# Kernel optimization log

Hardware: AMD Instinct MI355X
Metric: run time of the kernel (lower is better)

## Reference

```python
import jax, jax.numpy as jnp
import numpy as np

N = 100000      # nodes
E = 1600000     # edges
FX = 128        # raw node feature dim
MAXZ = 100      # z embedding / one-hot size
HID = 128       # hidden_channels
NL = 3          # num_layers
G = 512         # num graphs
BN_EPS = 1e-5


def _lin(key, din, dout):
    return jax.random.normal(key, (din, dout), jnp.float32) * (1.0 / np.sqrt(din))


def setup_inputs() -> dict:
    key = jax.random.key(0)
    ks = jax.random.split(key, 64)
    d = {}
    d["x"] = jax.random.normal(ks[0], (N, FX), jnp.float32)
    d["z"] = jax.random.randint(ks[1], (N,), 0, MAXZ)
    d["edge_index"] = jax.random.randint(ks[2], (2, E), 0, N)
    d["batch"] = jnp.sort(jax.random.randint(ks[3], (N,), 0, G))
    in0 = FX + 2 * MAXZ  # z_emb concatenated twice (faithful to source)
    ki = 4
    for l in range(NL):
        din = in0 if l == 0 else HID
        d[f"W1_{l}"] = _lin(ks[ki], din, HID); ki += 1
        d[f"b1_{l}"] = jnp.zeros((HID,), jnp.float32)
        d[f"W2_{l}"] = _lin(ks[ki], HID, HID); ki += 1
        d[f"b2_{l}"] = jnp.zeros((HID,), jnp.float32)
        d[f"g_{l}"] = jnp.ones((HID,), jnp.float32)
        d[f"be_{l}"] = jnp.zeros((HID,), jnp.float32)
    d["Wl1"] = _lin(ks[ki], NL * HID, HID); ki += 1
    d["bl1"] = jnp.zeros((HID,), jnp.float32)
    d["Wl2"] = _lin(ks[ki], HID, 1); ki += 1
    d["bl2"] = jnp.zeros((1,), jnp.float32)
    return d


def _gin_layer(h, src, dst, W1, b1, W2, b2, g, be):
    # GINConv with eps=0: nn(x + sum_{j->i} x_j)
    agg = jax.ops.segment_sum(h[src], dst, num_segments=N)  # [N, d]
    m = h + agg
    m = jax.nn.relu(m @ W1 + b1)
    m = jax.nn.relu(m @ W2 + b2)
    # training-mode BatchNorm1d over node axis (biased variance)
    mu = m.mean(0)
    var = jnp.mean((m - mu) ** 2, axis=0)
    return (m - mu) * jax.lax.rsqrt(var + BN_EPS) * g + be


def reference(x, z, edge_index, batch,
              W1_0, b1_0, W2_0, b2_0, g_0, be_0,
              W1_1, b1_1, W2_1, b2_1, g_1, be_1,
              W1_2, b1_2, W2_2, b2_2, g_2, be_2,
              Wl1, bl1, Wl2, bl2):
    src, dst = edge_index[0], edge_index[1]
    z_emb = jax.nn.one_hot(z, MAXZ, dtype=jnp.float32)  # [N, MAXZ]
    h = jnp.concatenate([z_emb, x], axis=1)
    h = jnp.concatenate([z_emb, h], axis=1)  # faithful double concat -> [N, FX+2*MAXZ]
    params = [(W1_0, b1_0, W2_0, b2_0, g_0, be_0),
              (W1_1, b1_1, W2_1, b2_1, g_1, be_1),
              (W1_2, b1_2, W2_2, b2_2, g_2, be_2)]
    xs = []
    for p in params:
        h = _gin_layer(h, src, dst, *p)
        xs.append(h)
    hcat = jnp.concatenate(xs, axis=1)  # jumping knowledge: [N, NL*HID]
    # global_mean_pool over graph ids
    counts = jax.ops.segment_sum(jnp.ones((N,), jnp.float32), batch, num_segments=G)
    pooled = jax.ops.segment_sum(hcat, batch, num_segments=G) / jnp.maximum(counts, 1.0)[:, None]
    out = jax.nn.relu(pooled @ Wl1 + bl1)
    # dropout is identity in eval / reference mode
    out = out @ Wl2 + bl2  # [G, 1]
    return out
```

## Files before the change

### kernel.cpp

```cpp
#include <hip/hip_runtime.h>
#include <hip/hip_bf16.h>

#define NN 100000
#define NROWS_PAD 100096
#define EE 1600000
#define GG 512
#define NPB 256
#define NB  ((NN + NPB - 1) / NPB)
#define CAP 5120
#define PCHUNK 4096
#define PBLOCKS ((EE + PCHUNK - 1) / PCHUNK)
#define SBANK 8
static constexpr float BN_EPS = 1e-5f;

typedef _Float16 half8 __attribute__((ext_vector_type(8)));
typedef float floatx4 __attribute__((ext_vector_type(4)));


__global__ __launch_bounds__(256) void k_part(const int* __restrict__ EI,
                                              int* __restrict__ bcursor,
                                              int* __restrict__ ebuf)
{
    __shared__ int h[NB];
    __shared__ int cur[NB];
    const int t = threadIdx.x;
    for (int i = t; i < NB; i += 256) h[i] = 0;
    __syncthreads();
    const int e0 = blockIdx.x * PCHUNK;
    const int e1 = (e0 + PCHUNK < EE) ? e0 + PCHUNK : EE;
    for (int e = e0 + t; e < e1; e += 256)
        atomicAdd(&h[EI[EE + e] >> 8], 1);
    __syncthreads();
    for (int i = t; i < NB; i += 256)
        cur[i] = h[i] ? (i * CAP + atomicAdd(&bcursor[i], h[i])) : 0;
    __syncthreads();
    for (int e = e0 + t; e < e1; e += 256) {
        int s = EI[e], d = EI[EE + e];
        int pos = atomicAdd(&cur[d >> 8], 1);
        ebuf[pos] = s | ((d & (NPB - 1)) << 17);
    }
}

__global__ __launch_bounds__(256) void k_csrbucket(const int* __restrict__ ebuf,
                                                   const int* __restrict__ bcursor,
                                                   int* __restrict__ rs,
                                                   int* __restrict__ re,
                                                   int* __restrict__ ssrc)
{
    __shared__ int cnt[NPB];
    __shared__ int cur[NPB];
    const int b = blockIdx.x, t = threadIdx.x;
    cnt[t] = 0;
    __syncthreads();
    const int e0 = b * CAP, e1 = e0 + bcursor[b];
    for (int e = e0 + t; e < e1; e += 256) {
        unsigned p = (unsigned)__builtin_nontemporal_load(&ebuf[e]);
        atomicAdd(&cnt[p >> 17], 1);
    }
    __syncthreads();
    int myc = cnt[t];
    for (int off = 1; off < 256; off <<= 1) {
        int u = (t >= off) ? cnt[t - off] : 0;
        __syncthreads();
        cnt[t] += u;
        __syncthreads();
    }
    int pos0 = e0 + cnt[t] - myc;
    int idx = b * NPB + t;
    if (idx < NN) { rs[idx] = pos0; re[idx] = pos0 + myc; }
    cur[t] = pos0;
    __syncthreads();
    for (int e = e0 + t; e < e1; e += 256) {
        unsigned p = (unsigned)__builtin_nontemporal_load(&ebuf[e]);
        int pos = atomicAdd(&cur[p >> 17], 1);
        ssrc[pos] = (int)(p & 0x1FFFFu);
    }
}


__global__ __launch_bounds__(512) void k_gstart(const int* __restrict__ batch,
                                                int* __restrict__ gstart)
{
    int g = threadIdx.x;
    int lo = 0, hi = NN;
    while (lo < hi) { int m = (lo + hi) >> 1; if (batch[m] < g) lo = m + 1; else hi = m; }
    gstart[g] = lo;
    if (g == 0) gstart[GG] = NN;
}


__device__ __forceinline__ void bn_fold(const float* __restrict__ statsL,
                                        const float* __restrict__ g,
                                        const float* __restrict__ be, int k,
                                        float& sc, float& sh)
{
    float cs = 0.f, cq = 0.f;
    #pragma unroll
    for (int b = 0; b < SBANK; ++b) {
        cs += statsL[b * 256 + k];
        cq += statsL[b * 256 + 128 + k];
    }
    float inv_n = 1.0f / (float)NN;
    float mu = cs * inv_n;
    float var = cq * inv_n - mu * mu;
    sc = g[k] * rsqrtf(var + BN_EPS);
    sh = be[k] - mu * sc;
}

__global__ __launch_bounds__(256) void k_prep(
    const float* __restrict__ W1, const float* __restrict__ W2,
    const float* __restrict__ statsPrev,
    const float* __restrict__ gP, const float* __restrict__ beP,
    _Float16* __restrict__ Wt1, _Float16* __restrict__ Wt2,
    float* __restrict__ cvec, int l)
{
    __shared__ float shs[128];
    int b = blockIdx.x, t = threadIdx.x;
    if (b < 64) {
        int idx = b * 256 + t;
        int n = idx >> 7, k = idx & 127;
        if (l == 0) {
            Wt1[idx] = (_Float16)W1[(200 + k) * 128 + n];
        } else {
            float sc, sh;
            bn_fold(statsPrev, gP, beP, k, sc, sh);
            Wt1[idx] = (_Float16)(sc * W1[k * 128 + n]);
        }
    } else if (b < 128) {
        int idx = (b - 64) * 256 + t;
        int n = idx >> 7, k = idx & 127;
        Wt2[idx] = (_Float16)W2[k * 128 + n];
    } else {
        if (t < 128) {
            float sc, sh = 0.f;
            if (l != 0) bn_fold(statsPrev, gP, beP, t, sc, sh);
            shs[t] = sh;
        }
        __syncthreads();
        if (t < 128) {
            float acc = 0.f;
            if (l != 0) {
                #pragma unroll 4
                for (int k = 0; k < 128; ++k)
                    acc = fmaf(shs[k], W1[k * 128 + t], acc);
            }
            cvec[t] = acc;
        }
    }
}


#define MM_CORE_G128(Ah, Wth)                                                \
    const int lane = tid & 63;                                               \
    const int wv = tid >> 6;                                                 \
    const int ml = lane & 15;                                                \
    const int quad = lane >> 4;                                              \
    const int wr = wv >> 1, wc = wv & 1;                                     \
    floatx4 acc[4][4];                                                       \
    for (int r = 0; r < 4; ++r)                                              \
        for (int t = 0; t < 4; ++t)                                          \
            acc[r][t] = (floatx4){0.f, 0.f, 0.f, 0.f};                       \
    {                                                                        \
        const size_t arb = (size_t)(row0 + 64 * wr + ml) * 128;              \
        _Pragma("unroll")                                                    \
        for (int kq = 0; kq < 4; ++kq) {                                     \
            int k0 = kq * 32;                                                \
            half8 a[4];                                                      \
            _Pragma("unroll")                                                \
            for (int r = 0; r < 4; ++r)                                      \
                a[r] = *(const half8*)&Ah[arb + (size_t)(16 * r) * 128 + k0 + quad * 8]; \
            _Pragma("unroll")                                                \
            for (int t = 0; t < 4; ++t) {                                    \
                half8 bf = *(const half8*)&Wth[(size_t)(64 * wc + 16 * t + ml) * 128 + k0 + quad * 8]; \
                _Pragma("unroll")                                            \
                for (int r = 0; r < 4; ++r)                                  \
                    acc[r][t] = __builtin_amdgcn_mfma_f32_16x16x32_f16(a[r], bf, acc[r][t], 0, 0, 0); \
            }                                                                \
        }                                                                    \
    }

#define MM_STORE_LDS128(Csh, Out)                                            \
    __syncthreads();                                                         \
    _Pragma("unroll")                                                        \
    for (int c = 0; c < 8; ++c) {                                            \
        int chunk = tid * 8 + c * 2048;                                      \
        if (row0 + (chunk >> 7) < NN)                                        \
            *(half8*)&Out[(size_t)row0 * 128 + chunk] = *(const half8*)&Csh[chunk]; \
    }

__global__ __launch_bounds__(256) void k_mm_embed(
    const float* __restrict__ X, const _Float16* __restrict__ Wth,
    const int* __restrict__ Z, const float* __restrict__ W1,
    _Float16* __restrict__ Ph)
{
    __shared__ _Float16 Csh[64 * 128];
    const int tid = threadIdx.x;
    const int row0 = blockIdx.x * 64;
    const int lane = tid & 63;
    const int wv = tid >> 6;
    const int ml = lane & 15;
    const int quad = lane >> 4;
    const int wr = wv >> 1, wc = wv & 1;
    floatx4 acc[2][4];
    #pragma unroll
    for (int r = 0; r < 2; ++r)
        #pragma unroll
        for (int t = 0; t < 4; ++t)
            acc[r][t] = (floatx4){0.f, 0.f, 0.f, 0.f};
    int r0g = row0 + 32 * wr + ml;
    int r1g = r0g + 16;
    if (r0g > NN - 1) r0g = NN - 1;
    if (r1g > NN - 1) r1g = NN - 1;
    const float* x0 = &X[(size_t)r0g * 128];
    const float* x1 = &X[(size_t)r1g * 128];
    #pragma unroll
    for (int kq = 0; kq < 4; ++kq) {
        int k0 = kq * 32 + quad * 8;
        float4 f0a = *(const float4*)&x0[k0];
        float4 f0b = *(const float4*)&x0[k0 + 4];
        float4 f1a = *(const float4*)&x1[k0];
        float4 f1b = *(const float4*)&x1[k0 + 4];
        half8 a0 = { (_Float16)f0a.x, (_Float16)f0a.y, (_Float16)f0a.z, (_Float16)f0a.w,
                     (_Float16)f0b.x, (_Float16)f0b.y, (_Float16)f0b.z, (_Float16)f0b.w };
        half8 a1 = { (_Float16)f1a.x, (_Float16)f1a.y, (_Float16)f1a.z, (_Float16)f1a.w,
                     (_Float16)f1b.x, (_Float16)f1b.y, (_Float16)f1b.z, (_Float16)f1b.w };
        #pragma unroll
        for (int t = 0; t < 4; ++t) {
            half8 bf = *(const half8*)&Wth[(size_t)(64 * wc + 16 * t + ml) * 128 + kq * 32 + quad * 8];
            acc[0][t] = __builtin_amdgcn_mfma_f32_16x16x32_f16(a0, bf, acc[0][t], 0, 0, 0);
            acc[1][t] = __builtin_amdgcn_mfma_f32_16x16x32_f16(a1, bf, acc[1][t], 0, 0, 0);
        }
    }
    #pragma unroll
    for (int r = 0; r < 2; ++r)
        #pragma unroll
        for (int j = 0; j < 4; ++j) {
            int lrow = 32 * wr + 16 * r + quad * 4 + j;
            int grow = row0 + lrow;
            int zv = (grow < NN) ? Z[grow] : 0;
            const float* w0 = &W1[zv * 128];
            const float* w1 = &W1[(100 + zv) * 128];
            #pragma unroll
            for (int t = 0; t < 4; ++t) {
                int gcol = 64 * wc + 16 * t + ml;
                Csh[lrow * 128 + gcol] = (_Float16)(acc[r][t][j] + w0[gcol] + w1[gcol]);
            }
        }
    __syncthreads();
    #pragma unroll
    for (int c = 0; c < 4; ++c) {
        int chunk = tid * 8 + c * 2048;
        if (row0 + (chunk >> 7) < NN)
            *(half8*)&Ph[(size_t)row0 * 128 + chunk] = *(const half8*)&Csh[chunk];
    }
}

__global__ __launch_bounds__(256) void k_mm1(
    const _Float16* __restrict__ Ah, const _Float16* __restrict__ Wth,
    _Float16* __restrict__ Ph)
{
    __shared__ _Float16 Csh[128 * 128];
    const int tid = threadIdx.x;
    const int row0 = blockIdx.x * 128;
    MM_CORE_G128(Ah, Wth)
    #pragma unroll
    for (int r = 0; r < 4; ++r)
        #pragma unroll
        for (int j = 0; j < 4; ++j) {
            int lrow = 64 * wr + 16 * r + quad * 4 + j;
            #pragma unroll
            for (int t = 0; t < 4; ++t)
                Csh[lrow * 128 + 64 * wc + 16 * t + ml] = (_Float16)acc[r][t][j];
        }
    MM_STORE_LDS128(Csh, Ph)
}

__global__ __launch_bounds__(256) void k_mm2(
    const _Float16* __restrict__ Ah, const _Float16* __restrict__ Wth,
    const float* __restrict__ b2, _Float16* __restrict__ Oh,
    float* __restrict__ statsL)
{
    __shared__ _Float16 Csh[128 * 128];
    __shared__ float cs[128];
    __shared__ float cq[128];
    const int tid = threadIdx.x;
    const int row0 = blockIdx.x * 128;
    if (tid < 128) { cs[tid] = 0.f; cq[tid] = 0.f; }
    __syncthreads();

    MM_CORE_G128(Ah, Wth)

    float b2v[4];
    #pragma unroll
    for (int t = 0; t < 4; ++t) b2v[t] = b2[64 * wc + 16 * t + ml];
    float st[4] = {0.f, 0.f, 0.f, 0.f};
    float qt[4] = {0.f, 0.f, 0.f, 0.f};
    #pragma unroll
    for (int r = 0; r < 4; ++r)
        #pragma unroll
        for (int j = 0; j < 4; ++j) {
            int lrow = 64 * wr + 16 * r + quad * 4 + j;
            bool ok = (row0 + lrow) < NN;
            #pragma unroll
            for (int t = 0; t < 4; ++t) {
                int gcol = 64 * wc + 16 * t + ml;
                float v = ok ? fmaxf(acc[r][t][j] + b2v[t], 0.f) : 0.f;
                Csh[lrow * 128 + gcol] = (_Float16)v;
                st[t] += v;
                qt[t] += v * v;
            }
        }
    #pragma unroll
    for (int t = 0; t < 4; ++t) {
        int gcol = 64 * wc + 16 * t + ml;
        atomicAdd(&cs[gcol], st[t]);
        atomicAdd(&cq[gcol], qt[t]);
    }
    MM_STORE_LDS128(Csh, Oh)
    if (tid < 128) {
        float* bank = statsL + (blockIdx.x & (SBANK - 1)) * 256;
        atomicAdd(&bank[tid], cs[tid]);
        atomicAdd(&bank[128 + tid], cq[tid]);
    }
}


__global__ __launch_bounds__(256) void k_aggregate(
    const _Float16* __restrict__ Ph, const int* __restrict__ rs,
    const int* __restrict__ re, const int* __restrict__ ssrc,
    const float* __restrict__ b1, const float* __restrict__ cvec,
    _Float16* __restrict__ Mh)
{
    int idx = blockIdx.x * 256 + threadIdx.x;
    int node = idx >> 4, q = idx & 15;
    if (node >= NN) return;
    int s0 = rs[node], s1 = re[node];
    float degp1 = (float)(s1 - s0 + 1);
    float acc[8];
    half8 pv = *(const half8*)&Ph[(size_t)node * 128 + q * 8];
    #pragma unroll
    for (int j = 0; j < 8; ++j)
        acc[j] = (float)pv[j] + fmaf(degp1, cvec[q * 8 + j], b1[q * 8 + j]);
    int e = s0;
    for (; e + 7 < s1; e += 8) {
        int sidx[8];
        #pragma unroll
        for (int u = 0; u < 8; ++u)
            sidx[u] = __builtin_nontemporal_load(&ssrc[e + u]);
        half8 v[8];
        #pragma unroll
        for (int u = 0; u < 8; ++u)
            v[u] = *(const half8*)&Ph[(size_t)sidx[u] * 128 + q * 8];
        #pragma unroll
        for (int j = 0; j < 8; ++j)
            acc[j] += (((float)v[0][j] + (float)v[1][j]) + ((float)v[2][j] + (float)v[3][j]))
                    + (((float)v[4][j] + (float)v[5][j]) + ((float)v[6][j] + (float)v[7][j]));
    }
    for (; e + 1 < s1; e += 2) {
        int sa = __builtin_nontemporal_load(&ssrc[e]);
        int sb = __builtin_nontemporal_load(&ssrc[e + 1]);
        half8 va = *(const half8*)&Ph[(size_t)sa * 128 + q * 8];
        half8 vb = *(const half8*)&Ph[(size_t)sb * 128 + q * 8];
        #pragma unroll
        for (int j = 0; j < 8; ++j) acc[j] += (float)va[j] + (float)vb[j];
    }
    if (e < s1) {
        int sa = __builtin_nontemporal_load(&ssrc[e]);
        half8 va = *(const half8*)&Ph[(size_t)sa * 128 + q * 8];
        #pragma unroll
        for (int j = 0; j < 8; ++j) acc[j] += (float)va[j];
    }
    half8 o;
    #pragma unroll
    for (int j = 0; j < 8; ++j) o[j] = (_Float16)fmaxf(acc[j], 0.f);
    __builtin_nontemporal_store(o, (half8*)&Mh[(size_t)node * 128 + q * 8]);
}


__global__ __launch_bounds__(256) void k_pool(
    const _Float16* __restrict__ Ah, const int* __restrict__ gstart,
    const float* __restrict__ statsL,
    const float* __restrict__ g_, const float* __restrict__ be,
    float* __restrict__ pooled, int loff)
{
    __shared__ float red[16][128];
    int g = blockIdx.x;
    int t = threadIdx.x;
    int rg = t >> 4, seg = t & 15;
    int s = gstart[g], e = gstart[g + 1];
    float acc[8] = {};
    for (int i = s + rg; i < e; i += 16) {
        half8 v = *(const half8*)&Ah[(size_t)i * 128 + seg * 8];
        #pragma unroll
        for (int j = 0; j < 8; ++j) acc[j] += (float)v[j];
    }
    #pragma unroll
    for (int j = 0; j < 8; ++j) red[rg][seg * 8 + j] = acc[j];
    __syncthreads();
    int cnt = e - s;
    float inv = 1.0f / (float)(cnt > 0 ? cnt : 1);
    if (t < 128) {
        float s_ = 0.f;
        #pragma unroll
        for (int r = 0; r < 16; ++r) s_ += red[r][t];
        float sc, sh;
        bn_fold(statsL, g_, be, t, sc, sh);
        pooled[g * 384 + loff + t] = fmaf(sc, s_ * inv, sh);
    }
}

__global__ __launch_bounds__(128) void k_final(
    const float* __restrict__ pooled,
    const float* __restrict__ Wl1, const float* __restrict__ bl1,
    const float* __restrict__ Wl2, const float* __restrict__ bl2,
    float* __restrict__ out)
{
    __shared__ float pr[384];
    __shared__ float red[128];
    int g = blockIdx.x, j = threadIdx.x;
    for (int i = j; i < 384; i += 128) pr[i] = pooled[g * 384 + i];
    __syncthreads();
    float acc = bl1[j];
    for (int k = 0; k < 384; ++k) acc = fmaf(pr[k], Wl1[k * 128 + j], acc);
    float r = fmaxf(acc, 0.f) * Wl2[j];
    red[j] = r;
    __syncthreads();
    for (int off = 64; off > 0; off >>= 1) {
        if (j < off) red[j] += red[j + off];
        __syncthreads();
    }
    if (j == 0) out[g] = red[0] + bl2[0];
}

extern "C" void kernel_launch(void* const* d_in, const int* in_sizes, int n_in,
                              void* d_out, int out_size, void* d_ws, size_t ws_size,
                              hipStream_t stream)
{
    const float* x     = (const float*)d_in[0];
    const int*   z     = (const int*)d_in[1];
    const int*   ei    = (const int*)d_in[2];
    const int*   batch = (const int*)d_in[3];
    const float* W1a[3] = {(const float*)d_in[4],  (const float*)d_in[10], (const float*)d_in[16]};
    const float* b1a[3] = {(const float*)d_in[5],  (const float*)d_in[11], (const float*)d_in[17]};
    const float* W2a[3] = {(const float*)d_in[6],  (const float*)d_in[12], (const float*)d_in[18]};
    const float* b2a[3] = {(const float*)d_in[7],  (const float*)d_in[13], (const float*)d_in[19]};
    const float* ga[3]  = {(const float*)d_in[8],  (const float*)d_in[14], (const float*)d_in[20]};
    const float* bea[3] = {(const float*)d_in[9],  (const float*)d_in[15], (const float*)d_in[21]};
    const float* Wl1 = (const float*)d_in[22];
    const float* bl1 = (const float*)d_in[23];
    const float* Wl2 = (const float*)d_in[24];
    const float* bl2 = (const float*)d_in[25];
    float* out = (float*)d_out;

    char* ws = (char*)d_ws;
    size_t off = 0;
    auto alloc = [&](size_t bytes) {
        void* p = ws + off;
        off += (bytes + 255) & ~(size_t)255;
        return p;
    };
    _Float16* Ph  = (_Float16*)alloc((size_t)NROWS_PAD * 128 * 2);
    _Float16* Mh  = (_Float16*)alloc((size_t)NROWS_PAD * 128 * 2);
    _Float16* Ahb = (_Float16*)alloc((size_t)NROWS_PAD * 128 * 2);
    _Float16* Wt1 = (_Float16*)alloc((size_t)128 * 128 * 2);
    _Float16* Wt2 = (_Float16*)alloc((size_t)128 * 128 * 2);
    int*   ebuf     = (int*)alloc((size_t)NB * CAP * 4);
    int*   ssrc     = (int*)alloc((size_t)NB * CAP * 4);
    int*   rs       = (int*)alloc((size_t)NN * 4);
    int*   re       = (int*)alloc((size_t)NN * 4);
    float* stats    = (float*)alloc((size_t)3 * SBANK * 256 * 4);
    int*   bcursor  = (int*)alloc((size_t)NB * 4);
    int*   gstart   = (int*)alloc((size_t)(GG + 1) * 4);
    float* cvec     = (float*)alloc(128 * 4);
    float* pooled   = (float*)alloc((size_t)GG * 384 * 4);

    const int embedBlocks = (NN + 63) / 64;
    const int mmBlocks    = (NN + 127) / 128;
    const int aggBlocks   = (NN * 16 + 255) / 256;

    hipMemsetAsync(stats, 0, (size_t)3 * SBANK * 256 * 4 + (size_t)NB * 4, stream);
    k_part<<<PBLOCKS, 256, 0, stream>>>(ei, bcursor, ebuf);
    k_gstart<<<1, 512, 0, stream>>>(batch, gstart);
    k_csrbucket<<<NB, 256, 0, stream>>>(ebuf, bcursor, rs, re, ssrc);

    const float* statsPrev = stats;
    for (int l = 0; l < 3; ++l) {
        float* statsL = stats + (size_t)l * SBANK * 256;
        const float* pg  = (l > 0) ? ga[l - 1] : ga[0];
        const float* pbe = (l > 0) ? bea[l - 1] : bea[0];
        k_prep<<<129, 256, 0, stream>>>(W1a[l], W2a[l], statsPrev, pg, pbe,
                                        Wt1, Wt2, cvec, l);
        if (l == 0)
            k_mm_embed<<<embedBlocks, 256, 0, stream>>>(x, Wt1, z, W1a[0], Ph);
        else
            k_mm1<<<mmBlocks, 256, 0, stream>>>(Ahb, Wt1, Ph);
        k_aggregate<<<aggBlocks, 256, 0, stream>>>(Ph, rs, re, ssrc, b1a[l], cvec, Mh);
        k_mm2<<<mmBlocks, 256, 0, stream>>>(Mh, Wt2, b2a[l], Ahb, statsL);
        k_pool<<<GG, 256, 0, stream>>>(Ahb, gstart, statsL, ga[l], bea[l],
                                       pooled, l * 128);
        statsPrev = statsL;
    }
    k_final<<<GG, 128, 0, stream>>>(pooled, Wl1, bl1, Wl2, bl2, out);
}
```

Before: 601.5 us.

## Fuse per-graph mean pooling into mm2 epilogue and fold BN in final kernel

Removes the separate per-layer pooling kernel: mm2 now accumulates raw per-graph column sums in shared memory, keyed by sorted batch ids, and flushes them with global atomics into a pre-zeroed buffer. BatchNorm scale/shift and the mean division are applied later in the final kernel, which is valid because the affine BN commutes with the mean. This saves a re-read of the activation matrix and a launch per layer. In exchange mm2 does many shared-memory atomics per element, which can contend heavily, and float atomic ordering makes the sums nondeterministic.

```diff
diff --git a/kernel.cpp b/kernel.cpp
--- a/kernel.cpp
+++ b/kernel.cpp
@@ -277,16 +277,24 @@
 
 __global__ __launch_bounds__(256) void k_mm2(
     const _Float16* __restrict__ Ah, const _Float16* __restrict__ Wth,
-    const float* __restrict__ b2, _Float16* __restrict__ Oh,
-    float* __restrict__ statsL)
+    const float* __restrict__ b2, const int* __restrict__ batch,
+    _Float16* __restrict__ Oh, float* __restrict__ statsL,
+    float* __restrict__ praw, int loff)
 {
     __shared__ _Float16 Csh[128 * 128];
     __shared__ float cs[128];
     __shared__ float cq[128];
+    __shared__ float pacc[8][128];
+    __shared__ int bsh[128];
+    __shared__ int used[8];
     const int tid = threadIdx.x;
     const int row0 = blockIdx.x * 128;
     if (tid < 128) { cs[tid] = 0.f; cq[tid] = 0.f; }
-    __syncthreads();
+    for (int i = tid; i < 8 * 128; i += 256) ((float*)pacc)[i] = 0.f;
+    if (tid < 8) used[tid] = 0;
+    if (tid < 128) bsh[tid] = (row0 + tid < NN) ? batch[row0 + tid] : -1;
+    __syncthreads();
+    const int g0 = bsh[0];
 
     MM_CORE_G128(Ah, Wth)
 
@@ -300,7 +308,9 @@
         #pragma unroll
         for (int j = 0; j < 4; ++j) {
             int lrow = 64 * wr + 16 * r + quad * 4 + j;
-            bool ok = (row0 + lrow) < NN;
+            int gg = bsh[lrow];
+            int li = gg - g0;
+            bool ok = gg >= 0;
             #pragma unroll
             for (int t = 0; t < 4; ++t) {
                 int gcol = 64 * wc + 16 * t + ml;
@@ -308,7 +318,12 @@
                 Csh[lrow * 128 + gcol] = (_Float16)v;
                 st[t] += v;
                 qt[t] += v * v;
+                if (ok) {
+                    if (li < 8) atomicAdd(&pacc[li][gcol], v);
+                    else        atomicAdd(&praw[(size_t)gg * 384 + loff + gcol], v);
+                }
             }
+            if (ok && li < 8) used[li] = 1;
         }
     #pragma unroll
     for (int t = 0; t < 4; ++t) {
@@ -317,6 +332,12 @@
         atomicAdd(&cq[gcol], qt[t]);
     }
     MM_STORE_LDS128(Csh, Oh)
+    {
+        int col = tid & 127;
+        for (int s = tid >> 7; s < 8; s += 2)
+            if (used[s])
+                atomicAdd(&praw[(size_t)(g0 + s) * 384 + loff + col], pacc[s][col]);
+    }
     if (tid < 128) {
         float* bank = statsL + (blockIdx.x & (SBANK - 1)) * 256;
         atomicAdd(&bank[tid], cs[tid]);
@@ -377,40 +398,12 @@
 }
 
 
-__global__ __launch_bounds__(256) void k_pool(
-    const _Float16* __restrict__ Ah, const int* __restrict__ gstart,
-    const float* __restrict__ statsL,
-    const float* __restrict__ g_, const float* __restrict__ be,
-    float* __restrict__ pooled, int loff)
-{
-    __shared__ float red[16][128];
-    int g = blockIdx.x;
-    int t = threadIdx.x;
-    int rg = t >> 4, seg = t & 15;
-    int s = gstart[g], e = gstart[g + 1];
-    float acc[8] = {};
-    for (int i = s + rg; i < e; i += 16) {
-        half8 v = *(const half8*)&Ah[(size_t)i * 128 + seg * 8];
-        #pragma unroll
-        for (int j = 0; j < 8; ++j) acc[j] += (float)v[j];
-    }
-    #pragma unroll
-    for (int j = 0; j < 8; ++j) red[rg][seg * 8 + j] = acc[j];
-    __syncthreads();
-    int cnt = e - s;
-    float inv = 1.0f / (float)(cnt > 0 ? cnt : 1);
-    if (t < 128) {
-        float s_ = 0.f;
-        #pragma unroll
-        for (int r = 0; r < 16; ++r) s_ += red[r][t];
-        float sc, sh;
-        bn_fold(statsL, g_, be, t, sc, sh);
-        pooled[g * 384 + loff + t] = fmaf(sc, s_ * inv, sh);
-    }
-}
-
 __global__ __launch_bounds__(128) void k_final(
-    const float* __restrict__ pooled,
+    const float* __restrict__ praw, const int* __restrict__ gstart,
+    const float* __restrict__ stats,
+    const float* __restrict__ g0p, const float* __restrict__ be0p,
+    const float* __restrict__ g1p, const float* __restrict__ be1p,
+    const float* __restrict__ g2p, const float* __restrict__ be2p,
     const float* __restrict__ Wl1, const float* __restrict__ bl1,
     const float* __restrict__ Wl2, const float* __restrict__ bl2,
     float* __restrict__ out)
@@ -418,7 +411,16 @@
     __shared__ float pr[384];
     __shared__ float red[128];
     int g = blockIdx.x, j = threadIdx.x;
-    for (int i = j; i < 384; i += 128) pr[i] = pooled[g * 384 + i];
+    int cnt = gstart[g + 1] - gstart[g];
+    float inv = 1.0f / (float)(cnt > 0 ? cnt : 1);
+    #pragma unroll
+    for (int l = 0; l < 3; ++l) {
+        const float* gp = (l == 0) ? g0p : (l == 1) ? g1p : g2p;
+        const float* bp = (l == 0) ? be0p : (l == 1) ? be1p : be2p;
+        float sc, sh;
+        bn_fold(stats + (size_t)l * SBANK * 256, gp, bp, j, sc, sh);
+        pr[l * 128 + j] = fmaf(sc, praw[g * 384 + l * 128 + j] * inv, sh);
+    }
     __syncthreads();
     float acc = bl1[j];
     for (int k = 0; k < 384; ++k) acc = fmaf(pr[k], Wl1[k * 128 + j], acc);
@@ -470,15 +472,16 @@
     int*   re       = (int*)alloc((size_t)NN * 4);
     float* stats    = (float*)alloc((size_t)3 * SBANK * 256 * 4);
     int*   bcursor  = (int*)alloc((size_t)NB * 4);
+    float* praw     = (float*)alloc((size_t)GG * 384 * 4);
     int*   gstart   = (int*)alloc((size_t)(GG + 1) * 4);
     float* cvec     = (float*)alloc(128 * 4);
-    float* pooled   = (float*)alloc((size_t)GG * 384 * 4);
 
     const int embedBlocks = (NN + 63) / 64;
     const int mmBlocks    = (NN + 127) / 128;
     const int aggBlocks   = (NN * 16 + 255) / 256;
 
-    hipMemsetAsync(stats, 0, (size_t)3 * SBANK * 256 * 4 + (size_t)NB * 4, stream);
+    size_t zlen = (size_t)((char*)(praw + (size_t)GG * 384) - (char*)stats);
+    hipMemsetAsync(stats, 0, zlen, stream);
     k_part<<<PBLOCKS, 256, 0, stream>>>(ei, bcursor, ebuf);
     k_gstart<<<1, 512, 0, stream>>>(batch, gstart);
     k_csrbucket<<<NB, 256, 0, stream>>>(ebuf, bcursor, rs, re, ssrc);
@@ -495,10 +498,11 @@
         else
             k_mm1<<<mmBlocks, 256, 0, stream>>>(Ahb, Wt1, Ph);
         k_aggregate<<<aggBlocks, 256, 0, stream>>>(Ph, rs, re, ssrc, b1a[l], cvec, Mh);
-        k_mm2<<<mmBlocks, 256, 0, stream>>>(Mh, Wt2, b2a[l], Ahb, statsL);
-        k_pool<<<GG, 256, 0, stream>>>(Ahb, gstart, statsL, ga[l], bea[l],
-                                       pooled, l * 128);
+        k_mm2<<<mmBlocks, 256, 0, stream>>>(Mh, Wt2, b2a[l], batch, Ahb, statsL,
+                                            praw, l * 128);
         statsPrev = statsL;
     }
-    k_final<<<GG, 128, 0, stream>>>(pooled, Wl1, bl1, Wl2, bl2, out);
-}
+    k_final<<<GG, 128, 0, stream>>>(praw, gstart, stats,
+                                    ga[0], bea[0], ga[1], bea[1], ga[2], bea[2],
+                                    Wl1, bl1, Wl2, bl2, out);
+}
```

After: 807.1 us. 34.2% more time.
